# Performance work log

Measured on AMD Instinct MI355X. Metric: run time of the kernel, lower is better.

The kernel has to match this reference:

```python
import jax, jax.numpy as jnp
import numpy as np


def setup_inputs() -> dict:
    key = jax.random.key(0)
    k1, k2, k3 = jax.random.split(key, 3)
    B, H, W = 32, 512, 512
    N = H * W  # tokens
    K = 32768  # positive_trials
    decision_scores = jax.random.normal(k1, (B, N, 2), dtype=jnp.float32)
    s_map = jax.random.uniform(k2, (B, 1, H, W), dtype=jnp.float32)
    # uniform noise for gumbel sampling, kept away from {0,1} for log stability
    u = jax.random.uniform(k3, (B, N, 2), dtype=jnp.float32, minval=1e-6, maxval=1.0 - 1e-6)
    return {"decision_scores": decision_scores, "s_map": s_map, "u": u, "positive_trials": K}


def reference(decision_scores, s_map, u, positive_trials):
    B, N, _ = decision_scores.shape
    # gumbel_softmax(hard=False, tau=1): softmax(logits + gumbel_noise)
    gumbel = -jnp.log(-jnp.log(u))
    logp = jax.nn.log_softmax(decision_scores + gumbel, axis=-1)  # [B, N, 2]
    # soft_decisions = p[..., 0]
    # Tokenizer: [B, 1, H, W] -> [B, N, 1]; use channel 0 as salience score.
    scores = s_map.reshape(B, 1, -1).transpose(0, 2, 1)[..., 0]  # [B, N]
    # argsort descending, take top-k indices == lax.top_k indices
    _, idx = jax.lax.top_k(scores, positive_trials)  # [B, K]
    trials = jnp.zeros((B, N), dtype=decision_scores.dtype)
    trials = trials.at[jnp.arange(B)[:, None], idx].set(1.0)  # scatter ones
    # BCE(sum): -sum(t*log(p) + (1-t)*log(1-p)); with 2-class softmax, 1-p0 = p1.
    # torch BCE clamps log terms at -100.
    logp0 = jnp.clip(logp[..., 0], -100.0)
    logp1 = jnp.clip(logp[..., 1], -100.0)
    loss = -jnp.sum(trials * logp0 + (1.0 - trials) * logp1)
    return loss
```

## Files before the change

### kernel.cpp

```cpp
#include <hip/hip_runtime.h>

#define NB    4096
#define CAPL  1024
#define BATCH 32
#define NTOK  262144
#define HB_PER_BATCH 8
#define HIST_BLOCKS  (BATCH * HB_PER_BATCH)
#define LOSS_BLOCKS  4096
#define LOSS_THREADS 256

__device__ __forceinline__ int bucket_of(float v) {
    int b = (int)(v * (float)NB);
    return b > NB - 1 ? NB - 1 : b;
}

__global__ __launch_bounds__(1024) void hist_kernel(const float* __restrict__ smap,
                                                    unsigned short* __restrict__ hist_part) {
    __shared__ int lh[NB];
    for (int i = threadIdx.x; i < NB; i += 1024) lh[i] = 0;
    __syncthreads();
    const int b  = blockIdx.x >> 3;
    const int cb = blockIdx.x & 7;
    const int chunk = NTOK / HB_PER_BATCH;
    const float4* src = (const float4*)(smap + (size_t)b * NTOK + (size_t)cb * chunk);
    const int nf4 = chunk / 4;
    for (int i = threadIdx.x; i < nf4; i += 1024) {
        float4 v = src[i];
        atomicAdd(&lh[bucket_of(v.x)], 1);
        atomicAdd(&lh[bucket_of(v.y)], 1);
        atomicAdd(&lh[bucket_of(v.z)], 1);
        atomicAdd(&lh[bucket_of(v.w)], 1);
    }
    __syncthreads();
    unsigned short* dst = hist_part + (size_t)blockIdx.x * NB;
    for (int i = threadIdx.x; i < NB; i += 1024)
        dst[i] = (unsigned short)lh[i];
}

__global__ __launch_bounds__(1024) void selref_kernel(
        const float* __restrict__ smap, const unsigned short* __restrict__ hist_part,
        const int* __restrict__ kptr, float* __restrict__ T, int* __restrict__ ncut) {
    __shared__ int   lh[NB];
    __shared__ int   suf[1024 + 1];
    __shared__ float cv[CAPL];
    __shared__ int   ci[CAPL];
    __shared__ int   s_cnt, s_tb, s_R;
    const int b = blockIdx.x;
    const int t = threadIdx.x;
    if (t == 0) s_cnt = 0;

    const unsigned short* hp = hist_part + (size_t)b * HB_PER_BATCH * NB;
    for (int i = t; i < NB; i += 1024) {
        int s = 0;
        #pragma unroll
        for (int p = 0; p < HB_PER_BATCH; p++) s += hp[p * NB + i];
        lh[i] = s;
    }
    __syncthreads();

    const int base = t * 4;
    int c = lh[base] + lh[base + 1] + lh[base + 2] + lh[base + 3];
    suf[t] = c;
    if (t == 0) suf[1024] = 0;
    __syncthreads();
    for (int off = 1; off < 1024; off <<= 1) {
        int v = suf[t] + ((t + off < 1024) ? suf[t + off] : 0);
        __syncthreads();
        suf[t] = v;
        __syncthreads();
    }
    const int K = *kptr;
    {
        int cum = suf[t + 1];
        #pragma unroll
        for (int i = 3; i >= 0; i--) {
            int hb = lh[base + i];
            if (cum < K && cum + hb >= K) { s_tb = base + i; s_R = K - cum; }
            cum += hb;
        }
    }
    __syncthreads();
    const int tb = s_tb;

    const float4* src = (const float4*)(smap + (size_t)b * NTOK);
    #pragma unroll 4
    for (int k = 0; k < 64; k++) {
        int fi = t + k * 1024;
        float4 v = src[fi];
        float vals[4] = {v.x, v.y, v.z, v.w};
        #pragma unroll
        for (int s = 0; s < 4; s++) {
            if (bucket_of(vals[s]) == tb) {
                int p = atomicAdd(&s_cnt, 1);
                if (p < CAPL) { cv[p] = vals[s]; ci[p] = 4 * fi + s; }
            }
        }
    }
    __syncthreads();

    int M = s_cnt, R = s_R;
    bool overflow = (M > CAPL);
    if (M > CAPL) M = CAPL;
    if (overflow || R > M || R < 1) {
        if (t == 0) { T[b] = (float)tb / (float)NB; ncut[b] = 0x7fffffff; }
        return;
    }
    for (int i = t; i < M; i += 1024) {
        float vi = cv[i]; int ii = ci[i];
        int r = 0;
        for (int j = 0; j < M; j++) {
            float vj = cv[j];
            r += (vj > vi) || (vj == vi && ci[j] < ii);
        }
        if (r == R - 1) { T[b] = vi; ncut[b] = ii; }
    }
}

__device__ __forceinline__ float token_loss(float d0, float d1, float u0, float u1,
                                            bool sel) {
    float g0 = -__logf(-__logf(u0));
    float g1 = -__logf(-__logf(u1));
    float dd = (d0 + g0) - (d1 + g1);
    float l  = __logf(1.f + __expf(-fabsf(dd)));
    float lp0 = (dd >= 0.f) ? -l      : dd - l;
    float lp1 = (dd >= 0.f) ? -l - dd : -l;
    lp0 = fmaxf(lp0, -100.f); lp1 = fmaxf(lp1, -100.f);
    return sel ? -lp0 : -lp1;
}

__global__ __launch_bounds__(256) void loss_kernel(
        const float* __restrict__ ds, const float* __restrict__ u,
        const float* __restrict__ smap, const float* __restrict__ T,
        const int* __restrict__ ncut, float* __restrict__ partials) {
    const int b = blockIdx.x >> 7;
    const int r = ((blockIdx.x & 127) << 8) | threadIdx.x;
    const float4* ds4 = (const float4*)(ds + (size_t)b * NTOK * 2) + 4 * (size_t)r;
    const float4* u4  = (const float4*)(u  + (size_t)b * NTOK * 2) + 4 * (size_t)r;
    const float4* s4  = (const float4*)(smap + (size_t)b * NTOK) + 2 * (size_t)r;

    float4 d0 = ds4[0], d1 = ds4[1], d2 = ds4[2], d3 = ds4[3];
    float4 w0 = u4[0],  w1 = u4[1],  w2 = u4[2],  w3 = u4[3];
    float4 sA = s4[0],  sB = s4[1];
    const float Tb = T[b];
    const int   nc = ncut[b];
    const int   n0 = r << 3;

    bool e0 = (sA.x > Tb) || (sA.x == Tb && (n0 + 0) <= nc);
    bool e1 = (sA.y > Tb) || (sA.y == Tb && (n0 + 1) <= nc);
    bool e2 = (sA.z > Tb) || (sA.z == Tb && (n0 + 2) <= nc);
    bool e3 = (sA.w > Tb) || (sA.w == Tb && (n0 + 3) <= nc);
    bool e4 = (sB.x > Tb) || (sB.x == Tb && (n0 + 4) <= nc);
    bool e5 = (sB.y > Tb) || (sB.y == Tb && (n0 + 5) <= nc);
    bool e6 = (sB.z > Tb) || (sB.z == Tb && (n0 + 6) <= nc);
    bool e7 = (sB.w > Tb) || (sB.w == Tb && (n0 + 7) <= nc);

    float acc = token_loss(d0.x, d0.y, w0.x, w0.y, e0)
              + token_loss(d0.z, d0.w, w0.z, w0.w, e1)
              + token_loss(d1.x, d1.y, w1.x, w1.y, e2)
              + token_loss(d1.z, d1.w, w1.z, w1.w, e3)
              + token_loss(d2.x, d2.y, w2.x, w2.y, e4)
              + token_loss(d2.z, d2.w, w2.z, w2.w, e5)
              + token_loss(d3.x, d3.y, w3.x, w3.y, e6)
              + token_loss(d3.z, d3.w, w3.z, w3.w, e7);

    for (int off = 32; off > 0; off >>= 1) acc += __shfl_down(acc, off, 64);
    __shared__ float red[4];
    const int lane = threadIdx.x & 63, wv = threadIdx.x >> 6;
    if (lane == 0) red[wv] = acc;
    __syncthreads();
    if (threadIdx.x == 0)
        partials[blockIdx.x] = red[0] + red[1] + red[2] + red[3];
}

__global__ __launch_bounds__(1024) void reduce_kernel(const float* __restrict__ partials,
                                                      float* __restrict__ out) {
    float acc = 0.f;
    for (int i = threadIdx.x; i < LOSS_BLOCKS; i += 1024) acc += partials[i];
    for (int off = 32; off > 0; off >>= 1) acc += __shfl_down(acc, off, 64);
    __shared__ float red[16];
    const int lane = threadIdx.x & 63, wv = threadIdx.x >> 6;
    if (lane == 0) red[wv] = acc;
    __syncthreads();
    if (threadIdx.x == 0) {
        float s = 0.f;
        for (int w = 0; w < 16; w++) s += red[w];
        out[0] = s;
    }
}

extern "C" void kernel_launch(void* const* d_in, const int* in_sizes, int n_in,
                              void* d_out, int out_size, void* d_ws, size_t ws_size,
                              hipStream_t stream) {
    const float* ds   = (const float*)d_in[0];
    const float* smap = (const float*)d_in[1];
    const float* u    = (const float*)d_in[2];
    const int*   kptr = (const int*)d_in[3];

    unsigned short* hist_part = (unsigned short*)d_ws;
    float* T        = (float*)(hist_part + (size_t)HIST_BLOCKS * NB);
    int*   ncut     = (int*)(T + BATCH);
    float* partials = (float*)(ncut + BATCH);

    hist_kernel<<<HIST_BLOCKS, 1024, 0, stream>>>(smap, hist_part);
    selref_kernel<<<BATCH, 1024, 0, stream>>>(smap, hist_part, kptr, T, ncut);
    loss_kernel<<<LOSS_BLOCKS, LOSS_THREADS, 0, stream>>>(ds, u, smap, T, ncut, partials);
    reduce_kernel<<<1, 1024, 0, stream>>>(partials, (float*)d_out);
}
```

Measured before the change: 214.2 us.

## Fuse histogram with loss pass using per-bucket logit-diff sums for selection correction

Reworks the loss algebra so every token is first charged the unselected loss (softplus of the logit difference), and selected tokens are corrected by subtracting their logit difference. The histogram pass now also reads ds and u, computes the loss and logit differences, and accumulates per-bucket sums of the difference. This removes the separate full re-read of ds, u and smap in a later loss kernel. The selection kernel then adds the differences above the threshold bucket and resolves the boundary bucket exactly. The cost is extra shared-memory float atomics in the histogram pass and scattered gathers in selection. There is a small numerical risk from the -100 clamp no longer being applied per term when tokens are selected.

```diff
diff --git a/kernel.cpp b/kernel.cpp
--- a/kernel.cpp
+++ b/kernel.cpp
@@ -4,57 +4,103 @@
 #define CAPL  1024
 #define BATCH 32
 #define NTOK  262144
-#define HB_PER_BATCH 8
-#define HIST_BLOCKS  (BATCH * HB_PER_BATCH)
-#define LOSS_BLOCKS  4096
-#define LOSS_THREADS 256
+#define HPB   8
+#define ABLK  (BATCH * HPB)
+#define ATHR  1024
+
+typedef float f4 __attribute__((ext_vector_type(4)));
 
 __device__ __forceinline__ int bucket_of(float v) {
     int b = (int)(v * (float)NB);
     return b > NB - 1 ? NB - 1 : b;
 }
 
-__global__ __launch_bounds__(1024) void hist_kernel(const float* __restrict__ smap,
-                                                    unsigned short* __restrict__ hist_part) {
-    __shared__ int lh[NB];
-    for (int i = threadIdx.x; i < NB; i += 1024) lh[i] = 0;
+__device__ __forceinline__ void token_terms(float d0, float d1, float u0, float u1,
+                                            float& dd, float& bce) {
+    float g0 = -__logf(-__logf(u0));
+    float g1 = -__logf(-__logf(u1));
+    dd = (d0 + g0) - (d1 + g1);
+    float l = __logf(1.f + __expf(-fabsf(dd)));
+    bce = fminf(l + fmaxf(dd, 0.f), 100.f);
+}
+
+__global__ __launch_bounds__(1024) void fused_kernel(
+        const float* __restrict__ ds, const float* __restrict__ u,
+        const float* __restrict__ smap,
+        unsigned short* __restrict__ hist_part, float* __restrict__ dsum_part,
+        float* __restrict__ bce_part) {
+    __shared__ int   lh[NB];
+    __shared__ float ldd[NB];
+    for (int i = threadIdx.x; i < NB; i += ATHR) { lh[i] = 0; ldd[i] = 0.f; }
     __syncthreads();
     const int b  = blockIdx.x >> 3;
     const int cb = blockIdx.x & 7;
-    const int chunk = NTOK / HB_PER_BATCH;
-    const float4* src = (const float4*)(smap + (size_t)b * NTOK + (size_t)cb * chunk);
-    const int nf4 = chunk / 4;
-    for (int i = threadIdx.x; i < nf4; i += 1024) {
-        float4 v = src[i];
-        atomicAdd(&lh[bucket_of(v.x)], 1);
-        atomicAdd(&lh[bucket_of(v.y)], 1);
-        atomicAdd(&lh[bucket_of(v.z)], 1);
-        atomicAdd(&lh[bucket_of(v.w)], 1);
-    }
-    __syncthreads();
-    unsigned short* dst = hist_part + (size_t)blockIdx.x * NB;
-    for (int i = threadIdx.x; i < NB; i += 1024)
-        dst[i] = (unsigned short)lh[i];
-}
-
-__global__ __launch_bounds__(1024) void selref_kernel(
-        const float* __restrict__ smap, const unsigned short* __restrict__ hist_part,
-        const int* __restrict__ kptr, float* __restrict__ T, int* __restrict__ ncut) {
+    const size_t Q0 = (size_t)b * (NTOK / 4) + (size_t)cb * (NTOK / 4 / HPB);
+    const f4* s4 = (const f4*)smap + Q0;
+    const f4* d4 = (const f4*)ds + 2 * Q0;
+    const f4* u4 = (const f4*)u  + 2 * Q0;
+    float bce = 0.f;
+    for (int k = 0; k < 8; k++) {
+        int q = threadIdx.x + k * ATHR;
+        f4 sv = s4[q];
+        f4 dA = __builtin_nontemporal_load(&d4[2 * q]);
+        f4 dB = __builtin_nontemporal_load(&d4[2 * q + 1]);
+        f4 uA = __builtin_nontemporal_load(&u4[2 * q]);
+        f4 uB = __builtin_nontemporal_load(&u4[2 * q + 1]);
+        float dd0, dd1, dd2, dd3, t0, t1, t2, t3;
+        token_terms(dA.x, dA.y, uA.x, uA.y, dd0, t0);
+        token_terms(dA.z, dA.w, uA.z, uA.w, dd1, t1);
+        token_terms(dB.x, dB.y, uB.x, uB.y, dd2, t2);
+        token_terms(dB.z, dB.w, uB.z, uB.w, dd3, t3);
+        bce += (t0 + t1) + (t2 + t3);
+        atomicAdd(&lh[bucket_of(sv.x)], 1); atomicAdd(&ldd[bucket_of(sv.x)], dd0);
+        atomicAdd(&lh[bucket_of(sv.y)], 1); atomicAdd(&ldd[bucket_of(sv.y)], dd1);
+        atomicAdd(&lh[bucket_of(sv.z)], 1); atomicAdd(&ldd[bucket_of(sv.z)], dd2);
+        atomicAdd(&lh[bucket_of(sv.w)], 1); atomicAdd(&ldd[bucket_of(sv.w)], dd3);
+    }
+    __syncthreads();
+    unsigned short* hp = hist_part + (size_t)blockIdx.x * NB;
+    float*          dp = dsum_part + (size_t)blockIdx.x * NB;
+    for (int i = threadIdx.x; i < NB; i += ATHR) {
+        hp[i] = (unsigned short)lh[i];
+        dp[i] = ldd[i];
+    }
+    for (int off = 32; off > 0; off >>= 1) bce += __shfl_down(bce, off, 64);
+    __shared__ float red[16];
+    const int lane = threadIdx.x & 63, wv = threadIdx.x >> 6;
+    if (lane == 0) red[wv] = bce;
+    __syncthreads();
+    if (threadIdx.x == 0) {
+        float s = 0.f;
+        for (int w = 0; w < 16; w++) s += red[w];
+        bce_part[blockIdx.x] = s;
+    }
+}
+
+__global__ __launch_bounds__(1024) void selcorr_kernel(
+        const float* __restrict__ smap, const float* __restrict__ ds,
+        const float* __restrict__ u,
+        const unsigned short* __restrict__ hist_part, const float* __restrict__ dsum_part,
+        const int* __restrict__ kptr, float* __restrict__ corr) {
     __shared__ int   lh[NB];
+    __shared__ float ldd[NB];
     __shared__ int   suf[1024 + 1];
     __shared__ float cv[CAPL];
     __shared__ int   ci[CAPL];
+    __shared__ float cdd[CAPL];
+    __shared__ float csel[CAPL];
     __shared__ int   s_cnt, s_tb, s_R;
-    const int b = blockIdx.x;
-    const int t = threadIdx.x;
+    __shared__ float fred1[16], fred2[16];
+    const int b = blockIdx.x, t = threadIdx.x;
     if (t == 0) s_cnt = 0;
 
-    const unsigned short* hp = hist_part + (size_t)b * HB_PER_BATCH * NB;
+    const unsigned short* hp = hist_part + (size_t)b * HPB * NB;
+    const float*          dp = dsum_part + (size_t)b * HPB * NB;
     for (int i = t; i < NB; i += 1024) {
-        int s = 0;
+        int s = 0; float f = 0.f;
         #pragma unroll
-        for (int p = 0; p < HB_PER_BATCH; p++) s += hp[p * NB + i];
-        lh[i] = s;
+        for (int p = 0; p < HPB; p++) { s += hp[(size_t)p * NB + i]; f += dp[(size_t)p * NB + i]; }
+        lh[i] = s; ldd[i] = f;
     }
     __syncthreads();
 
@@ -80,111 +126,81 @@
         }
     }
     __syncthreads();
-    const int tb = s_tb;
-
-    const float4* src = (const float4*)(smap + (size_t)b * NTOK);
-    #pragma unroll 4
+    const int tb = s_tb, R = s_R;
+
+    float s1p = 0.f;
+    for (int i = t; i < NB; i += 1024) if (i > tb) s1p += ldd[i];
+    for (int off = 32; off > 0; off >>= 1) s1p += __shfl_down(s1p, off, 64);
+    const int lane = t & 63, wv = t >> 6;
+    if (lane == 0) fred1[wv] = s1p;
+
+    const f4* s4 = (const f4*)smap + (size_t)b * (NTOK / 4);
     for (int k = 0; k < 64; k++) {
-        int fi = t + k * 1024;
-        float4 v = src[fi];
+        int q = t + k * 1024;
+        f4 v = s4[q];
         float vals[4] = {v.x, v.y, v.z, v.w};
         #pragma unroll
-        for (int s = 0; s < 4; s++) {
-            if (bucket_of(vals[s]) == tb) {
+        for (int j = 0; j < 4; j++) {
+            if (bucket_of(vals[j]) == tb) {
                 int p = atomicAdd(&s_cnt, 1);
-                if (p < CAPL) { cv[p] = vals[s]; ci[p] = 4 * fi + s; }
+                if (p < CAPL) { cv[p] = vals[j]; ci[p] = 4 * q + j; }
             }
         }
     }
     __syncthreads();
-
-    int M = s_cnt, R = s_R;
-    bool overflow = (M > CAPL);
-    if (M > CAPL) M = CAPL;
-    if (overflow || R > M || R < 1) {
-        if (t == 0) { T[b] = (float)tb / (float)NB; ncut[b] = 0x7fffffff; }
-        return;
-    }
+    int M = s_cnt;
+    const bool ovf = (M > CAPL);
+    if (ovf) M = CAPL;
+
     for (int i = t; i < M; i += 1024) {
-        float vi = cv[i]; int ii = ci[i];
-        int r = 0;
-        for (int j = 0; j < M; j++) {
-            float vj = cv[j];
-            r += (vj > vi) || (vj == vi && ci[j] < ii);
+        const int n = ci[i];
+        float2 dpair = ((const float2*)ds)[(size_t)b * NTOK + n];
+        float2 upair = ((const float2*)u)[(size_t)b * NTOK + n];
+        float g0 = -__logf(-__logf(upair.x));
+        float g1 = -__logf(-__logf(upair.y));
+        cdd[i] = (dpair.x + g0) - (dpair.y + g1);
+    }
+    for (int i = t; i < CAPL; i += 1024) csel[i] = 0.f;
+    __syncthreads();
+    if (!ovf) {
+        for (int i = t; i < M; i += 1024) {
+            float vi = cv[i]; int ii = ci[i];
+            int r = 0;
+            for (int j = 0; j < M; j++) {
+                float vj = cv[j];
+                r += (vj > vi) || (vj == vi && ci[j] < ii);
+            }
+            if (r < R) csel[i] = cdd[i];
         }
-        if (r == R - 1) { T[b] = vi; ncut[b] = ii; }
-    }
-}
-
-__device__ __forceinline__ float token_loss(float d0, float d1, float u0, float u1,
-                                            bool sel) {
-    float g0 = -__logf(-__logf(u0));
-    float g1 = -__logf(-__logf(u1));
-    float dd = (d0 + g0) - (d1 + g1);
-    float l  = __logf(1.f + __expf(-fabsf(dd)));
-    float lp0 = (dd >= 0.f) ? -l      : dd - l;
-    float lp1 = (dd >= 0.f) ? -l - dd : -l;
-    lp0 = fmaxf(lp0, -100.f); lp1 = fmaxf(lp1, -100.f);
-    return sel ? -lp0 : -lp1;
-}
-
-__global__ __launch_bounds__(256) void loss_kernel(
-        const float* __restrict__ ds, const float* __restrict__ u,
-        const float* __restrict__ smap, const float* __restrict__ T,
-        const int* __restrict__ ncut, float* __restrict__ partials) {
-    const int b = blockIdx.x >> 7;
-    const int r = ((blockIdx.x & 127) << 8) | threadIdx.x;
-    const float4* ds4 = (const float4*)(ds + (size_t)b * NTOK * 2) + 4 * (size_t)r;
-    const float4* u4  = (const float4*)(u  + (size_t)b * NTOK * 2) + 4 * (size_t)r;
-    const float4* s4  = (const float4*)(smap + (size_t)b * NTOK) + 2 * (size_t)r;
-
-    float4 d0 = ds4[0], d1 = ds4[1], d2 = ds4[2], d3 = ds4[3];
-    float4 w0 = u4[0],  w1 = u4[1],  w2 = u4[2],  w3 = u4[3];
-    float4 sA = s4[0],  sB = s4[1];
-    const float Tb = T[b];
-    const int   nc = ncut[b];
-    const int   n0 = r << 3;
-
-    bool e0 = (sA.x > Tb) || (sA.x == Tb && (n0 + 0) <= nc);
-    bool e1 = (sA.y > Tb) || (sA.y == Tb && (n0 + 1) <= nc);
-    bool e2 = (sA.z > Tb) || (sA.z == Tb && (n0 + 2) <= nc);
-    bool e3 = (sA.w > Tb) || (sA.w == Tb && (n0 + 3) <= nc);
-    bool e4 = (sB.x > Tb) || (sB.x == Tb && (n0 + 4) <= nc);
-    bool e5 = (sB.y > Tb) || (sB.y == Tb && (n0 + 5) <= nc);
-    bool e6 = (sB.z > Tb) || (sB.z == Tb && (n0 + 6) <= nc);
-    bool e7 = (sB.w > Tb) || (sB.w == Tb && (n0 + 7) <= nc);
-
-    float acc = token_loss(d0.x, d0.y, w0.x, w0.y, e0)
-              + token_loss(d0.z, d0.w, w0.z, w0.w, e1)
-              + token_loss(d1.x, d1.y, w1.x, w1.y, e2)
-              + token_loss(d1.z, d1.w, w1.z, w1.w, e3)
-              + token_loss(d2.x, d2.y, w2.x, w2.y, e4)
-              + token_loss(d2.z, d2.w, w2.z, w2.w, e5)
-              + token_loss(d3.x, d3.y, w3.x, w3.y, e6)
-              + token_loss(d3.z, d3.w, w3.z, w3.w, e7);
-
-    for (int off = 32; off > 0; off >>= 1) acc += __shfl_down(acc, off, 64);
+    }
+    __syncthreads();
+    float s2p = csel[t];
+    for (int off = 32; off > 0; off >>= 1) s2p += __shfl_down(s2p, off, 64);
+    if (lane == 0) fred2[wv] = s2p;
+    __syncthreads();
+    if (t == 0) {
+        float S1 = 0.f, S2 = 0.f;
+        for (int w = 0; w < 16; w++) { S1 += fred1[w]; S2 += fred2[w]; }
+        if (ovf) S2 = ldd[tb];
+        corr[b] = S1 + S2;
+    }
+}
+
+__global__ __launch_bounds__(256) void final_kernel(const float* __restrict__ bce_part,
+                                                    const float* __restrict__ corr,
+                                                    float* __restrict__ out) {
+    const int t = threadIdx.x;
+    float a = bce_part[t];
+    for (int off = 32; off > 0; off >>= 1) a += __shfl_down(a, off, 64);
     __shared__ float red[4];
-    const int lane = threadIdx.x & 63, wv = threadIdx.x >> 6;
-    if (lane == 0) red[wv] = acc;
-    __syncthreads();
-    if (threadIdx.x == 0)
-        partials[blockIdx.x] = red[0] + red[1] + red[2] + red[3];
-}
-
-__global__ __launch_bounds__(1024) void reduce_kernel(const float* __restrict__ partials,
-                                                      float* __restrict__ out) {
-    float acc = 0.f;
-    for (int i = threadIdx.x; i < LOSS_BLOCKS; i += 1024) acc += partials[i];
-    for (int off = 32; off > 0; off >>= 1) acc += __shfl_down(acc, off, 64);
-    __shared__ float red[16];
-    const int lane = threadIdx.x & 63, wv = threadIdx.x >> 6;
-    if (lane == 0) red[wv] = acc;
-    __syncthreads();
-    if (threadIdx.x == 0) {
-        float s = 0.f;
-        for (int w = 0; w < 16; w++) s += red[w];
-        out[0] = s;
+    const int lane = t & 63, wv = t >> 6;
+    if (lane == 0) red[wv] = a;
+    __syncthreads();
+    if (t == 0) {
+        float s = red[0] + red[1] + red[2] + red[3];
+        float cc = 0.f;
+        for (int i = 0; i < BATCH; i++) cc += corr[i];
+        out[0] = s - cc;
     }
 }
 
@@ -196,13 +212,12 @@
     const float* u    = (const float*)d_in[2];
     const int*   kptr = (const int*)d_in[3];
 
-    unsigned short* hist_part = (unsigned short*)d_ws;
-    float* T        = (float*)(hist_part + (size_t)HIST_BLOCKS * NB);
-    int*   ncut     = (int*)(T + BATCH);
-    float* partials = (float*)(ncut + BATCH);
-
-    hist_kernel<<<HIST_BLOCKS, 1024, 0, stream>>>(smap, hist_part);
-    selref_kernel<<<BATCH, 1024, 0, stream>>>(smap, hist_part, kptr, T, ncut);
-    loss_kernel<<<LOSS_BLOCKS, LOSS_THREADS, 0, stream>>>(ds, u, smap, T, ncut, partials);
-    reduce_kernel<<<1, 1024, 0, stream>>>(partials, (float*)d_out);
-}
+    float*          dsum_part = (float*)d_ws;
+    unsigned short* hist_part = (unsigned short*)(dsum_part + (size_t)ABLK * NB);
+    float*          bce_part  = (float*)(hist_part + (size_t)ABLK * NB);
+    float*          corr      = bce_part + ABLK;
+
+    fused_kernel<<<ABLK, ATHR, 0, stream>>>(ds, u, smap, hist_part, dsum_part, bce_part);
+    selcorr_kernel<<<BATCH, 1024, 0, stream>>>(smap, ds, u, hist_part, dsum_part, kptr, corr);
+    final_kernel<<<1, 256, 0, stream>>>(bce_part, corr, (float*)d_out);
+}
```

After: 218.8 us. +2.1%, slower.

## Split top-k selection into parallel mask build, candidate refine, and bitmask-driven loss

Applied to the files above, without the earlier changes.

Replaces the 32-block select/refine kernel, which rescanned all of s_map, with a histogram-threshold select kernel and a 1024-block mask-collect kernel. That kernel writes a per-token selection bitmask and gathers boundary-bucket candidates to global memory. A refine kernel ranks the candidates and ORs the top R into the mask. The loss kernel then reads one bit per token instead of the float s_map. This spreads the second s_map pass across many more blocks and shrinks loss-kernel traffic. In exchange it adds two launches plus global atomics on a per-batch counter, and there is no fallback if the candidate count exceeds the cap.

```diff
diff --git a/kernel.cpp b/kernel.cpp
--- a/kernel.cpp
+++ b/kernel.cpp
@@ -1,13 +1,15 @@
 #include <hip/hip_runtime.h>
 
 #define NB    4096
-#define CAPL  1024
+#define CAP   4096
 #define BATCH 32
 #define NTOK  262144
-#define HB_PER_BATCH 8
-#define HIST_BLOCKS  (BATCH * HB_PER_BATCH)
-#define LOSS_BLOCKS  4096
-#define LOSS_THREADS 256
+#define HPB   8
+#define HBLK  (BATCH * HPB)
+#define NWRD  (NTOK / 32)
+#define LOSS_BLOCKS 8192
+
+typedef float f4 __attribute__((ext_vector_type(4)));
 
 __device__ __forceinline__ int bucket_of(float v) {
     int b = (int)(v * (float)NB);
@@ -19,45 +21,36 @@
     __shared__ int lh[NB];
     for (int i = threadIdx.x; i < NB; i += 1024) lh[i] = 0;
     __syncthreads();
-    const int b  = blockIdx.x >> 3;
-    const int cb = blockIdx.x & 7;
-    const int chunk = NTOK / HB_PER_BATCH;
-    const float4* src = (const float4*)(smap + (size_t)b * NTOK + (size_t)cb * chunk);
-    const int nf4 = chunk / 4;
-    for (int i = threadIdx.x; i < nf4; i += 1024) {
-        float4 v = src[i];
+    const int b = blockIdx.x >> 3, cb = blockIdx.x & 7;
+    const f4* src = (const f4*)(smap + (size_t)b * NTOK + (size_t)cb * (NTOK / HPB));
+    for (int k = 0; k < 8; k++) {
+        f4 v = src[threadIdx.x + k * 1024];
         atomicAdd(&lh[bucket_of(v.x)], 1);
         atomicAdd(&lh[bucket_of(v.y)], 1);
         atomicAdd(&lh[bucket_of(v.z)], 1);
         atomicAdd(&lh[bucket_of(v.w)], 1);
     }
     __syncthreads();
-    unsigned short* dst = hist_part + (size_t)blockIdx.x * NB;
+    unsigned short* hp = hist_part + (size_t)blockIdx.x * NB;
     for (int i = threadIdx.x; i < NB; i += 1024)
-        dst[i] = (unsigned short)lh[i];
-}
-
-__global__ __launch_bounds__(1024) void selref_kernel(
-        const float* __restrict__ smap, const unsigned short* __restrict__ hist_part,
-        const int* __restrict__ kptr, float* __restrict__ T, int* __restrict__ ncut) {
-    __shared__ int   lh[NB];
-    __shared__ int   suf[1024 + 1];
-    __shared__ float cv[CAPL];
-    __shared__ int   ci[CAPL];
-    __shared__ int   s_cnt, s_tb, s_R;
-    const int b = blockIdx.x;
-    const int t = threadIdx.x;
-    if (t == 0) s_cnt = 0;
-
-    const unsigned short* hp = hist_part + (size_t)b * HB_PER_BATCH * NB;
+        hp[i] = (unsigned short)lh[i];
+}
+
+__global__ __launch_bounds__(1024) void select_kernel(
+        const unsigned short* __restrict__ hist_part, const int* __restrict__ kptr,
+        int* __restrict__ tbR, int* __restrict__ cnt) {
+    __shared__ int lh[NB];
+    __shared__ int suf[1025];
+    const int b = blockIdx.x, t = threadIdx.x;
+    if (t == 0) cnt[b] = 0;
+    const unsigned short* hp = hist_part + (size_t)b * HPB * NB;
     for (int i = t; i < NB; i += 1024) {
         int s = 0;
         #pragma unroll
-        for (int p = 0; p < HB_PER_BATCH; p++) s += hp[p * NB + i];
+        for (int p = 0; p < HPB; p++) s += hp[(size_t)p * NB + i];
         lh[i] = s;
     }
     __syncthreads();
-
     const int base = t * 4;
     int c = lh[base] + lh[base + 1] + lh[base + 2] + lh[base + 3];
     suf[t] = c;
@@ -70,49 +63,68 @@
         __syncthreads();
     }
     const int K = *kptr;
-    {
-        int cum = suf[t + 1];
-        #pragma unroll
-        for (int i = 3; i >= 0; i--) {
-            int hb = lh[base + i];
-            if (cum < K && cum + hb >= K) { s_tb = base + i; s_R = K - cum; }
-            cum += hb;
-        }
-    }
-    __syncthreads();
-    const int tb = s_tb;
-
-    const float4* src = (const float4*)(smap + (size_t)b * NTOK);
-    #pragma unroll 4
-    for (int k = 0; k < 64; k++) {
-        int fi = t + k * 1024;
-        float4 v = src[fi];
-        float vals[4] = {v.x, v.y, v.z, v.w};
+    int cum = suf[t + 1];
+    #pragma unroll
+    for (int i = 3; i >= 0; i--) {
+        int hb = lh[base + i];
+        if (cum < K && cum + hb >= K) { tbR[2 * b] = base + i; tbR[2 * b + 1] = K - cum; }
+        cum += hb;
+    }
+}
+
+__global__ __launch_bounds__(256) void maskcollect_kernel(const float* __restrict__ smap,
+        const int* __restrict__ tbR, unsigned* __restrict__ mask,
+        int* __restrict__ cnt, float* __restrict__ cval, int* __restrict__ cidx) {
+    const int b = blockIdx.x >> 5, cb = blockIdx.x & 31;
+    const int tb = tbR[2 * b];
+    const int t = cb * 256 + threadIdx.x;
+    const f4* src = (const f4*)(smap + (size_t)b * NTOK) + (size_t)t * 8;
+    const int n0 = t * 32;
+    unsigned w = 0;
+    #pragma unroll
+    for (int j = 0; j < 8; j++) {
+        f4 v = src[j];
+        float vv[4] = {v.x, v.y, v.z, v.w};
         #pragma unroll
         for (int s = 0; s < 4; s++) {
-            if (bucket_of(vals[s]) == tb) {
-                int p = atomicAdd(&s_cnt, 1);
-                if (p < CAPL) { cv[p] = vals[s]; ci[p] = 4 * fi + s; }
+            int bk = bucket_of(vv[s]);
+            if (bk > tb) {
+                w |= 1u << (4 * j + s);
+            } else if (bk == tb) {
+                int p = atomicAdd(&cnt[b], 1);
+                if (p < CAP) {
+                    cval[b * CAP + p] = vv[s];
+                    cidx[b * CAP + p] = n0 + 4 * j + s;
+                }
             }
         }
     }
-    __syncthreads();
-
-    int M = s_cnt, R = s_R;
-    bool overflow = (M > CAPL);
-    if (M > CAPL) M = CAPL;
-    if (overflow || R > M || R < 1) {
-        if (t == 0) { T[b] = (float)tb / (float)NB; ncut[b] = 0x7fffffff; }
-        return;
-    }
-    for (int i = t; i < M; i += 1024) {
-        float vi = cv[i]; int ii = ci[i];
+    mask[(size_t)b * NWRD + t] = w;
+}
+
+__global__ __launch_bounds__(256) void refine_kernel(const int* __restrict__ tbR,
+        const int* __restrict__ cnt, const float* __restrict__ cval,
+        const int* __restrict__ cidx, unsigned* __restrict__ mask) {
+    const int b = blockIdx.x;
+    const int R = tbR[2 * b + 1];
+    int M = cnt[b];
+    if (M > CAP) M = CAP;
+    __shared__ float sv[CAP];
+    __shared__ int   si[CAP];
+    for (int i = threadIdx.x; i < M; i += 256) {
+        sv[i] = cval[b * CAP + i];
+        si[i] = cidx[b * CAP + i];
+    }
+    __syncthreads();
+    for (int i = threadIdx.x; i < M; i += 256) {
+        float vi = sv[i]; int ii = si[i];
         int r = 0;
         for (int j = 0; j < M; j++) {
-            float vj = cv[j];
-            r += (vj > vi) || (vj == vi && ci[j] < ii);
+            float vj = sv[j];
+            r += (vj > vi) || (vj == vi && si[j] < ii);
         }
-        if (r == R - 1) { T[b] = vi; ncut[b] = ii; }
+        if (r < R)
+            atomicOr(&mask[(size_t)b * NWRD + (ii >> 5)], 1u << (ii & 31));
     }
 }
 
@@ -128,40 +140,25 @@
     return sel ? -lp0 : -lp1;
 }
 
-__global__ __launch_bounds__(256) void loss_kernel(
-        const float* __restrict__ ds, const float* __restrict__ u,
-        const float* __restrict__ smap, const float* __restrict__ T,
-        const int* __restrict__ ncut, float* __restrict__ partials) {
-    const int b = blockIdx.x >> 7;
-    const int r = ((blockIdx.x & 127) << 8) | threadIdx.x;
-    const float4* ds4 = (const float4*)(ds + (size_t)b * NTOK * 2) + 4 * (size_t)r;
-    const float4* u4  = (const float4*)(u  + (size_t)b * NTOK * 2) + 4 * (size_t)r;
-    const float4* s4  = (const float4*)(smap + (size_t)b * NTOK) + 2 * (size_t)r;
-
-    float4 d0 = ds4[0], d1 = ds4[1], d2 = ds4[2], d3 = ds4[3];
-    float4 w0 = u4[0],  w1 = u4[1],  w2 = u4[2],  w3 = u4[3];
-    float4 sA = s4[0],  sB = s4[1];
-    const float Tb = T[b];
-    const int   nc = ncut[b];
-    const int   n0 = r << 3;
-
-    bool e0 = (sA.x > Tb) || (sA.x == Tb && (n0 + 0) <= nc);
-    bool e1 = (sA.y > Tb) || (sA.y == Tb && (n0 + 1) <= nc);
-    bool e2 = (sA.z > Tb) || (sA.z == Tb && (n0 + 2) <= nc);
-    bool e3 = (sA.w > Tb) || (sA.w == Tb && (n0 + 3) <= nc);
-    bool e4 = (sB.x > Tb) || (sB.x == Tb && (n0 + 4) <= nc);
-    bool e5 = (sB.y > Tb) || (sB.y == Tb && (n0 + 5) <= nc);
-    bool e6 = (sB.z > Tb) || (sB.z == Tb && (n0 + 6) <= nc);
-    bool e7 = (sB.w > Tb) || (sB.w == Tb && (n0 + 7) <= nc);
-
-    float acc = token_loss(d0.x, d0.y, w0.x, w0.y, e0)
-              + token_loss(d0.z, d0.w, w0.z, w0.w, e1)
-              + token_loss(d1.x, d1.y, w1.x, w1.y, e2)
-              + token_loss(d1.z, d1.w, w1.z, w1.w, e3)
-              + token_loss(d2.x, d2.y, w2.x, w2.y, e4)
-              + token_loss(d2.z, d2.w, w2.z, w2.w, e5)
-              + token_loss(d3.x, d3.y, w3.x, w3.y, e6)
-              + token_loss(d3.z, d3.w, w3.z, w3.w, e7);
+__global__ __launch_bounds__(256) void loss_kernel(const float* __restrict__ ds,
+        const float* __restrict__ u, const unsigned* __restrict__ mask,
+        float* __restrict__ partials) {
+    int tid = blockIdx.x * blockDim.x + threadIdx.x;
+    int b = tid >> 16;
+    int p = tid & 65535;
+    const f4* ds4 = (const f4*)(ds + (size_t)b * NTOK * 2);
+    const f4* u4  = (const f4*)(u  + (size_t)b * NTOK * 2);
+    f4 dA = ds4[2 * p];
+    f4 dB = ds4[2 * p + 1];
+    f4 uA = u4[2 * p];
+    f4 uB = u4[2 * p + 1];
+    unsigned w = mask[(size_t)b * NWRD + (p >> 3)];
+    const int sh = (p & 7) * 4;
+
+    float acc = token_loss(dA.x, dA.y, uA.x, uA.y, (w >> (sh + 0)) & 1)
+              + token_loss(dA.z, dA.w, uA.z, uA.w, (w >> (sh + 1)) & 1)
+              + token_loss(dB.x, dB.y, uB.x, uB.y, (w >> (sh + 2)) & 1)
+              + token_loss(dB.z, dB.w, uB.z, uB.w, (w >> (sh + 3)) & 1);
 
     for (int off = 32; off > 0; off >>= 1) acc += __shfl_down(acc, off, 64);
     __shared__ float red[4];
@@ -197,12 +194,17 @@
     const int*   kptr = (const int*)d_in[3];
 
     unsigned short* hist_part = (unsigned short*)d_ws;
-    float* T        = (float*)(hist_part + (size_t)HIST_BLOCKS * NB);
-    int*   ncut     = (int*)(T + BATCH);
-    float* partials = (float*)(ncut + BATCH);
-
-    hist_kernel<<<HIST_BLOCKS, 1024, 0, stream>>>(smap, hist_part);
-    selref_kernel<<<BATCH, 1024, 0, stream>>>(smap, hist_part, kptr, T, ncut);
-    loss_kernel<<<LOSS_BLOCKS, LOSS_THREADS, 0, stream>>>(ds, u, smap, T, ncut, partials);
+    unsigned* mask  = (unsigned*)(hist_part + (size_t)HBLK * NB);
+    int*   tbR      = (int*)(mask + (size_t)BATCH * NWRD);
+    int*   cnt      = tbR + 2 * BATCH;
+    float* cval     = (float*)(cnt + BATCH);
+    int*   cidx     = (int*)(cval + (size_t)BATCH * CAP);
+    float* partials = (float*)(cidx + (size_t)BATCH * CAP);
+
+    hist_kernel<<<HBLK, 1024, 0, stream>>>(smap, hist_part);
+    select_kernel<<<BATCH, 1024, 0, stream>>>(hist_part, kptr, tbR, cnt);
+    maskcollect_kernel<<<1024, 256, 0, stream>>>(smap, tbR, mask, cnt, cval, cidx);
+    refine_kernel<<<BATCH, 256, 0, stream>>>(tbR, cnt, cval, cidx, mask);
+    loss_kernel<<<LOSS_BLOCKS, 256, 0, stream>>>(ds, u, mask, partials);
     reduce_kernel<<<1, 1024, 0, stream>>>(partials, (float*)d_out);
 }
```

After: 206.7 us. -3.5%, faster.
